# Optimization experiments

Hardware: AMD Instinct MI355X
Metric: run time of the kernel (lower is better)

## Reference

```python
import jax, jax.numpy as jnp
import numpy as np

B, N = 2, 512
D_NODE, D_EDGE, D_HID, H = 128, 64, 128, 8
DH = D_HID // H  # per-head dim = 16
SCALE = 1.0 / (D_HID ** 0.5)  # note: scale uses full d_hid as in source


def setup_inputs() -> dict:
    key = jax.random.key(0)
    k1, k2, k3, k4 = jax.random.split(key, 4)
    node_features = jax.random.normal(k1, (B, N, D_NODE), dtype=jnp.float32)
    edge_features = jax.random.normal(k2, (B, N, N, D_EDGE), dtype=jnp.float32)
    mask = jnp.ones((B, N, N), dtype=bool)
    # Linear weights (stored as (in, out); math identical to torch x @ W.T)
    W_node = jax.random.normal(k3, (D_NODE, 3 * D_HID), dtype=jnp.float32) / np.sqrt(D_NODE)
    W_edge = jax.random.normal(k4, (D_EDGE, 3 * D_HID), dtype=jnp.float32) / np.sqrt(D_EDGE)
    return {"node_features": node_features, "edge_features": edge_features,
            "mask": mask, "W_node": W_node, "W_edge": W_edge}


def _split_heads_node(x):
    # (b, n, h*c) -> (b, h, n, c)
    b, n, hc = x.shape
    return x.reshape(b, n, H, hc // H).transpose(0, 2, 1, 3)


def _split_heads_edge(x):
    # (b, n, m, h*c) -> (b, h, n, m, c)
    b, n, m, hc = x.shape
    return x.reshape(b, n, m, H, hc // H).transpose(0, 3, 1, 2, 4)


def reference(node_features, edge_features, mask, W_node, W_edge):
    # node qkv: (b, n, 3*d_hid) -> (b, h, n, 3*dh) -> chunk
    qkv_n = _split_heads_node(node_features @ W_node)
    q_node, k_node, v_node = jnp.split(qkv_n, 3, axis=-1)  # each (b,h,n,dh)
    # edge qkv: (b, n, n, 3*d_hid) -> (b, h, n, n, 3*dh) -> chunk
    qkv_e = _split_heads_edge(edge_features @ W_edge)
    q_edge, k_edge, v_edge = jnp.split(qkv_e, 3, axis=-1)  # each (b,h,n,n,dh)

    q = q_node[:, :, :, None, :] + q_edge   # (b,h,i,j,dh)
    k = k_node[:, :, None, :, :] + k_edge   # (b,h,i,j,dh)
    v = v_node[:, :, None, :, :] + v_edge   # (b,h,i,j,dh)

    dots = SCALE * jnp.einsum('bhijd,bhijd->bhij', q, k)
    attn = jax.nn.softmax(dots, axis=-1)
    out = jnp.einsum('bhij,bhijd->bhid', attn, v)  # (b,h,n,dh)
    # (b,h,n,dh) -> (b,n,h*dh)
    b, h, n, dh = out.shape
    return out.transpose(0, 2, 1, 3).reshape(b, n, h * dh)
```

## Files before the change

kernel.cpp:

```cpp
#include <hip/hip_runtime.h>
#include <hip/hip_bf16.h>

#define NN 512
#define OC 384
#define S2F 0.12751694f

typedef __attribute__((ext_vector_type(8))) short short8;
typedef __attribute__((ext_vector_type(4))) float f32x4;

#define LD4(p) (*reinterpret_cast<const f32x4*>(p))

__device__ __forceinline__ unsigned short f2bf(float x) {
    unsigned u = __builtin_bit_cast(unsigned, x);
    u = (u + 0x7fffu + ((u >> 16) & 1u)) >> 16;
    return (unsigned short)u;
}

__device__ __forceinline__ ushort4 cvt4(f32x4 a) {
    union { ushort4 u4; __hip_bfloat162 h[2]; } r;
    r.h[0] = __float22bfloat162_rn(make_float2(a[0], a[1]));
    r.h[1] = __float22bfloat162_rn(make_float2(a[2], a[3]));
    return r.u4;
}

__global__ __launch_bounds__(256) void prep0_kernel(
    const float* __restrict__ Wn, const float* __restrict__ We,
    const float* __restrict__ node,
    unsigned short* __restrict__ WtN, unsigned short* __restrict__ WtE,
    unsigned short* __restrict__ nodeBf)
{
    int idx = blockIdx.x * 256 + threadIdx.x;
    if (idx < 24576) {
        int o = idx >> 6, k = idx & 63;
        WtE[idx] = f2bf(We[k * OC + o]);
    } else if (idx < 24576 + 49152) {
        int id = idx - 24576;
        int o = id >> 7, k = id & 127;
        WtN[id] = f2bf(Wn[k * OC + o]);
    } else {
        int id = idx - 73728;
        nodeBf[id] = f2bf(node[id]);
    }
}

__global__ __launch_bounds__(256) void prep1_kernel(
    const unsigned short* __restrict__ nodeBf,
    const unsigned short* __restrict__ WtN,
    float* __restrict__ qnF,
    float* __restrict__ nodeKV)
{
    const int t = threadIdx.x;
    const int w = t >> 6;
    const int lane = t & 63;
    const int lj = lane & 15;
    const int quad = lane >> 4;
    const int nbase = blockIdx.x * 32;

    short8 bfr[2][4];
#pragma unroll
    for (int nt = 0; nt < 2; ++nt)
#pragma unroll
        for (int ks = 0; ks < 4; ++ks)
            bfr[nt][ks] = *reinterpret_cast<const short8*>(
                nodeBf + (size_t)(nbase + nt * 16 + lj) * 128 + ks * 32 + quad * 8);

#pragma unroll
    for (int m = 0; m < 6; ++m) {
        int ot = (6 * w + m) * 16;
        short8 afr[4];
#pragma unroll
        for (int ks = 0; ks < 4; ++ks)
            afr[ks] = *reinterpret_cast<const short8*>(
                WtN + (size_t)(ot + lj) * 128 + ks * 32 + quad * 8);
#pragma unroll
        for (int nt = 0; nt < 2; ++nt) {
            f32x4 acc = {0.f, 0.f, 0.f, 0.f};
#pragma unroll
            for (int ks = 0; ks < 4; ++ks)
                acc = __builtin_amdgcn_mfma_f32_16x16x32_bf16(afr[ks], bfr[nt][ks], acc, 0, 0, 0);
            int n = nbase + nt * 16 + lj;
            int bb = n >> 9, ii = n & 511;
#pragma unroll
            for (int r = 0; r < 4; ++r) {
                int o = ot + quad * 4 + r;
                int h = o / 48, rem = o - h * 48;
                if (rem < 16) {
                    qnF[((size_t)(bb * 8 + h) * NN + ii) * 16 + rem] = acc[r];
                } else {
                    int d = (rem - 16) & 15;
                    int kv = (rem >= 32) ? 1 : 0;
                    size_t slot = ((((size_t)(bb * 8 + h) * 4 + (d >> 2)) * 2 + kv) * NN + ii) * 4 + (d & 3);
                    nodeKV[slot] = acc[r];
                }
            }
        }
    }
}

__global__ __launch_bounds__(512, 2) void rt_attn_main(
    const float* __restrict__ edge,
    const float* __restrict__ qnF,
    const float* __restrict__ nodeKV,
    const unsigned short* __restrict__ WtE,
    float* __restrict__ oaP,
    float* __restrict__ lP)
{
    __shared__ unsigned short sE[2][64 * 72];
    const int blk = blockIdx.x;
    const int jt = blk & 7;
    const int ic = (blk >> 3) & 127;
    const int b  = blk >> 10;
    const int i0 = ic * 4;
    const int t = threadIdx.x;
    const int h = t >> 6;
    const int lane = t & 63;
    const int lj = lane & 15;
    const int quad = lane >> 4;

    const int sj0 = t >> 4;
    const int sj1 = sj0 + 32;
    const int sc = (t & 15) * 4;

    const float* eB = edge + ((size_t)(b * NN + i0) * NN + jt * 64) * 64;
    f32x4 pf0 = LD4(eB + (size_t)sj0 * 64 + sc);
    f32x4 pf1 = LD4(eB + (size_t)sj1 * 64 + sc);

    short8 afr[3][2];
#pragma unroll
    for (int T = 0; T < 3; ++T)
#pragma unroll
        for (int sec = 0; sec < 2; ++sec)
            afr[T][sec] = *reinterpret_cast<const short8*>(
                WtE + (size_t)(h * 48 + T * 16 + lj) * 64 + sec * 32 + quad * 8);

    const float* kvB = nodeKV + ((size_t)(b * 8 + h) * 4 + quad) * (2 * NN * 4) + (size_t)lj * 4;
    f32x4 ka[4], va[4];
#pragma unroll
    for (int jn = 0; jn < 4; ++jn) {
        const float* kvp = kvB + (size_t)(jt * 64 + jn * 16) * 4;
        ka[jn] = LD4(kvp);
        va[jn] = LD4(kvp + NN * 4);
    }

    const float* qB = qnF + ((size_t)(b * 8 + h) * NN + i0) * 16 + quad * 4;
    f32x4 qnC = LD4(qB);

    {
        *reinterpret_cast<ushort4*>(&sE[0][sj0 * 72 + sc]) = cvt4(pf0);
        *reinterpret_cast<ushort4*>(&sE[0][sj1 * 72 + sc]) = cvt4(pf1);
    }
    __syncthreads();

#pragma unroll
    for (int ii = 0; ii < 4; ++ii) {
        const int cur = ii & 1;
        f32x4 qnN;
        if (ii < 3) {
            const float* nb = eB + (size_t)(ii + 1) * (NN * 64);
            pf0 = LD4(nb + (size_t)sj0 * 64 + sc);
            pf1 = LD4(nb + (size_t)sj1 * 64 + sc);
            qnN = LD4(qB + (ii + 1) * 16);
        }
        float dp[4];
        f32x4 fvv[4];
#pragma unroll
        for (int jn = 0; jn < 4; ++jn) {
            const int jrow = jn * 16 + lj;
            short8 b0 = *reinterpret_cast<const short8*>(&sE[cur][jrow * 72 + quad * 8]);
            short8 b1 = *reinterpret_cast<const short8*>(&sE[cur][jrow * 72 + 32 + quad * 8]);
            f32x4 fq = qnC;
            fq = __builtin_amdgcn_mfma_f32_16x16x32_bf16(afr[0][0], b0, fq, 0, 0, 0);
            fq = __builtin_amdgcn_mfma_f32_16x16x32_bf16(afr[0][1], b1, fq, 0, 0, 0);
            f32x4 fk = ka[jn];
            fk = __builtin_amdgcn_mfma_f32_16x16x32_bf16(afr[1][0], b0, fk, 0, 0, 0);
            fk = __builtin_amdgcn_mfma_f32_16x16x32_bf16(afr[1][1], b1, fk, 0, 0, 0);
            f32x4 fv = va[jn];
            fv = __builtin_amdgcn_mfma_f32_16x16x32_bf16(afr[2][0], b0, fv, 0, 0, 0);
            fv = __builtin_amdgcn_mfma_f32_16x16x32_bf16(afr[2][1], b1, fv, 0, 0, 0);
            fvv[jn] = fv;
            float d0 = fq[0] * fk[0];
            d0 = fmaf(fq[1], fk[1], d0);
            d0 = fmaf(fq[2], fk[2], d0);
            d0 = fmaf(fq[3], fk[3], d0);
            dp[jn] = d0;
        }
        float t16[4], t32[4], wg[4];
        float l = 0.f;
#pragma unroll
        for (int jn = 0; jn < 4; ++jn) t16[jn] = __shfl_xor(dp[jn], 16);
#pragma unroll
        for (int jn = 0; jn < 4; ++jn) dp[jn] += t16[jn];
#pragma unroll
        for (int jn = 0; jn < 4; ++jn) t32[jn] = __shfl_xor(dp[jn], 32);
#pragma unroll
        for (int jn = 0; jn < 4; ++jn) {
            wg[jn] = exp2f((dp[jn] + t32[jn]) * S2F);
            l += wg[jn];
        }
        float oa[4] = {0.f, 0.f, 0.f, 0.f};
#pragma unroll
        for (int jn = 0; jn < 4; ++jn)
#pragma unroll
            for (int r = 0; r < 4; ++r)
                oa[r] = fmaf(wg[jn], fvv[jn][r], oa[r]);
#pragma unroll
        for (int off = 1; off <= 8; off <<= 1) {
            l += __shfl_xor(l, off);
#pragma unroll
            for (int r = 0; r < 4; ++r) oa[r] += __shfl_xor(oa[r], off);
        }
        if (lj == 0) {
            size_t pbase = ((size_t)(b * 8 + h) * 8 + jt) * NN + (i0 + ii);
            f32x4 o4;
#pragma unroll
            for (int r = 0; r < 4; ++r) o4[r] = oa[r];
            *reinterpret_cast<f32x4*>(oaP + pbase * 16 + quad * 4) = o4;
            if (quad == 0) lP[pbase] = l;
        }
        if (ii < 3) {
            *reinterpret_cast<ushort4*>(&sE[cur ^ 1][sj0 * 72 + sc]) = cvt4(pf0);
            *reinterpret_cast<ushort4*>(&sE[cur ^ 1][sj1 * 72 + sc]) = cvt4(pf1);
            __syncthreads();
            qnC = qnN;
        }
    }
}

__global__ __launch_bounds__(256) void combine_kernel(
    const float* __restrict__ oaP,
    const float* __restrict__ lP,
    float* __restrict__ out)
{
    int tid = blockIdx.x * 256 + threadIdx.x;
    int d = tid & 15;
    int i = (tid >> 4) & 511;
    int h = (tid >> 13) & 7;
    int b = tid >> 16;
    float num = 0.f, den = 0.f;
#pragma unroll
    for (int jt = 0; jt < 8; ++jt) {
        size_t pb = ((size_t)(b * 8 + h) * 8 + jt) * NN + i;
        num += oaP[pb * 16 + d];
        den += lP[pb];
    }
    out[((size_t)b * NN + i) * 128 + h * 16 + d] = num / den;
}

extern "C" void kernel_launch(void* const* d_in, const int* in_sizes, int n_in,
                              void* d_out, int out_size, void* d_ws, size_t ws_size,
                              hipStream_t stream) {
    const float* node = (const float*)d_in[0];
    const float* edge = (const float*)d_in[1];
    const float* Wn = (const float*)d_in[3];
    const float* We = (const float*)d_in[4];
    float* out = (float*)d_out;

    char* ws = (char*)d_ws;
    float* qnF = (float*)ws;
    float* nodeKV = (float*)(ws + 524288);
    unsigned short* WtE = (unsigned short*)(ws + 1572864);
    unsigned short* WtN = (unsigned short*)(ws + 1622016);
    unsigned short* nodeBf = (unsigned short*)(ws + 1720320);
    float* oaP = (float*)(ws + 2097152);
    float* lP  = (float*)(ws + 6291456);

    prep0_kernel<<<800, 256, 0, stream>>>(Wn, We, node, WtN, WtE, nodeBf);
    prep1_kernel<<<32, 256, 0, stream>>>(nodeBf, WtN, qnF, nodeKV);
    rt_attn_main<<<2 * 128 * 8, 512, 0, stream>>>(edge, qnF, nodeKV, WtE, oaP, lP);
    combine_kernel<<<512, 256, 0, stream>>>(oaP, lP, out);
}
```

Before: 232.8 us.

## Stage all edge rows into LDS via direct global-to-LDS loads, drop per-step syncs

The main attention kernel now issues asynchronous global_load_lds copies of all four i-rows of the fp32 edge tile into LDS at once. It uses a rotated (swizzled) column layout to avoid bank conflicts and converts to bf16 when reading the MFMA operands. This replaces the register-staged double buffer, the per-iteration conversion stores and the __syncthreads between rows, and raises the occupancy hint to 4 blocks. The trade is a 64KB LDS footprint per block, which may stop the higher occupancy from being reached, plus redundant bf16 conversions across heads.

```diff
diff --git a/kernel.cpp b/kernel.cpp
--- a/kernel.cpp
+++ b/kernel.cpp
@@ -16,11 +16,20 @@
     return (unsigned short)u;
 }
 
-__device__ __forceinline__ ushort4 cvt4(f32x4 a) {
-    union { ushort4 u4; __hip_bfloat162 h[2]; } r;
+__device__ __forceinline__ short8 cvt8(f32x4 a, f32x4 b) {
+    union { short8 s8; __hip_bfloat162 h[4]; } r;
     r.h[0] = __float22bfloat162_rn(make_float2(a[0], a[1]));
     r.h[1] = __float22bfloat162_rn(make_float2(a[2], a[3]));
-    return r.u4;
+    r.h[2] = __float22bfloat162_rn(make_float2(b[0], b[1]));
+    r.h[3] = __float22bfloat162_rn(make_float2(b[2], b[3]));
+    return r.s8;
+}
+
+__device__ __forceinline__ void gl_lds16(const float* g, float* l) {
+    __builtin_amdgcn_global_load_lds(
+        (const __attribute__((address_space(1))) void*)g,
+        (__attribute__((address_space(3))) void*)l,
+        16, 0, 0);
 }
 
 __global__ __launch_bounds__(256) void prep0_kernel(
@@ -97,7 +106,7 @@
     }
 }
 
-__global__ __launch_bounds__(512, 2) void rt_attn_main(
+__global__ __launch_bounds__(512, 4) void rt_attn_main(
     const float* __restrict__ edge,
     const float* __restrict__ qnF,
     const float* __restrict__ nodeKV,
@@ -105,7 +114,7 @@
     float* __restrict__ oaP,
     float* __restrict__ lP)
 {
-    __shared__ unsigned short sE[2][64 * 72];
+    __shared__ __align__(16) float sE[4 * 64 * 64];
     const int blk = blockIdx.x;
     const int jt = blk & 7;
     const int ic = (blk >> 3) & 127;
@@ -117,21 +126,21 @@
     const int lj = lane & 15;
     const int quad = lane >> 4;
 
-    const int sj0 = t >> 4;
-    const int sj1 = sj0 + 32;
-    const int sc = (t & 15) * 4;
-
-    const float* eB = edge + ((size_t)(b * NN + i0) * NN + jt * 64) * 64;
-    f32x4 pf0 = LD4(eB + (size_t)sj0 * 64 + sc);
-    f32x4 pf1 = LD4(eB + (size_t)sj1 * 64 + sc);
-
-    short8 afr[3][2];
-#pragma unroll
-    for (int T = 0; T < 3; ++T)
-#pragma unroll
-        for (int sec = 0; sec < 2; ++sec)
-            afr[T][sec] = *reinterpret_cast<const short8*>(
-                WtE + (size_t)(h * 48 + T * 16 + lj) * 64 + sec * 32 + quad * 8);
+    {
+        const int rL = lane >> 4;
+        const int cP = lane & 15;
+#pragma unroll
+        for (int m = 0; m < 8; ++m) {
+            const int chunk = h * 8 + m;
+            const int T  = chunk >> 4;
+            const int r0 = (chunk & 15) * 4;
+            const int r  = r0 + rL;
+            const int cl = (cP - r) & 15;
+            const float* src = edge
+                + ((size_t)(b * NN + i0 + T) * NN + jt * 64 + r) * 64 + cl * 4;
+            gl_lds16(src, &sE[chunk * 256]);
+        }
+    }
 
     const float* kvB = nodeKV + ((size_t)(b * 8 + h) * 4 + quad) * (2 * NN * 4) + (size_t)lj * 4;
     f32x4 ka[4], va[4];
@@ -142,32 +151,36 @@
         va[jn] = LD4(kvp + NN * 4);
     }
 
+    short8 afr[3][2];
+#pragma unroll
+    for (int T = 0; T < 3; ++T)
+#pragma unroll
+        for (int sec = 0; sec < 2; ++sec)
+            afr[T][sec] = *reinterpret_cast<const short8*>(
+                WtE + (size_t)(h * 48 + T * 16 + lj) * 64 + sec * 32 + quad * 8);
+
     const float* qB = qnF + ((size_t)(b * 8 + h) * NN + i0) * 16 + quad * 4;
     f32x4 qnC = LD4(qB);
 
-    {
-        *reinterpret_cast<ushort4*>(&sE[0][sj0 * 72 + sc]) = cvt4(pf0);
-        *reinterpret_cast<ushort4*>(&sE[0][sj1 * 72 + sc]) = cvt4(pf1);
-    }
+    const int po0 = (((2 * quad)     + lj) & 15) * 4;
+    const int po1 = (((2 * quad + 1) + lj) & 15) * 4;
+    const int po2 = (((2 * quad + 8) + lj) & 15) * 4;
+    const int po3 = (((2 * quad + 9) + lj) & 15) * 4;
+
+    asm volatile("s_waitcnt vmcnt(0)" ::: "memory");
     __syncthreads();
 
 #pragma unroll
     for (int ii = 0; ii < 4; ++ii) {
-        const int cur = ii & 1;
         f32x4 qnN;
-        if (ii < 3) {
-            const float* nb = eB + (size_t)(ii + 1) * (NN * 64);
-            pf0 = LD4(nb + (size_t)sj0 * 64 + sc);
-            pf1 = LD4(nb + (size_t)sj1 * 64 + sc);
-            qnN = LD4(qB + (ii + 1) * 16);
-        }
+        if (ii < 3) qnN = LD4(qB + (ii + 1) * 16);
         float dp[4];
         f32x4 fvv[4];
 #pragma unroll
         for (int jn = 0; jn < 4; ++jn) {
-            const int jrow = jn * 16 + lj;
-            short8 b0 = *reinterpret_cast<const short8*>(&sE[cur][jrow * 72 + quad * 8]);
-            short8 b1 = *reinterpret_cast<const short8*>(&sE[cur][jrow * 72 + 32 + quad * 8]);
+            const float* rb = &sE[ii * 4096 + (jn * 16 + lj) * 64];
+            short8 b0 = cvt8(LD4(rb + po0), LD4(rb + po1));
+            short8 b1 = cvt8(LD4(rb + po2), LD4(rb + po3));
             f32x4 fq = qnC;
             fq = __builtin_amdgcn_mfma_f32_16x16x32_bf16(afr[0][0], b0, fq, 0, 0, 0);
             fq = __builtin_amdgcn_mfma_f32_16x16x32_bf16(afr[0][1], b1, fq, 0, 0, 0);
@@ -217,12 +230,7 @@
             *reinterpret_cast<f32x4*>(oaP + pbase * 16 + quad * 4) = o4;
             if (quad == 0) lP[pbase] = l;
         }
-        if (ii < 3) {
-            *reinterpret_cast<ushort4*>(&sE[cur ^ 1][sj0 * 72 + sc]) = cvt4(pf0);
-            *reinterpret_cast<ushort4*>(&sE[cur ^ 1][sj1 * 72 + sc]) = cvt4(pf1);
-            __syncthreads();
-            qnC = qnN;
-        }
+        qnC = qnN;
     }
 }
 
```

Result: slower. 240.8 us (+3.4%).
